# Performance work log

Measured on AMD Instinct MI355X. Metric: run time of the kernel, lower is better.

The kernel has to match this reference:

```python
import jax, jax.numpy as jnp
import numpy as np

B, S, H, C = 256, 256, 768, 150  # batch, seq_len, hidden_size, total class prototypes


def setup_inputs() -> dict:
    key = jax.random.key(0)
    k1, k2, k3 = jax.random.split(key, 3)
    last_hidden_state = jax.random.normal(k1, (B, S, H), dtype=jnp.float32)
    attention_mask = jnp.ones((B, S), dtype=jnp.int32)
    means = jax.random.normal(k2, (C, H), dtype=jnp.float32)
    A = jax.random.normal(k3, (H, H), dtype=jnp.float32) / np.sqrt(H)
    # symmetric PSD-ish inverse-covariance, like pinv of a covariance (hermitian)
    cov_inv = A @ A.T + jnp.eye(H, dtype=jnp.float32)
    return {"last_hidden_state": last_hidden_state, "attention_mask": attention_mask,
            "means": means, "cov_inv": cov_inv}


def reference(last_hidden_state, attention_mask, means, cov_inv):
    # mean pooling over valid tokens: [B, S, H] -> [B, H]
    m = attention_mask[..., None].astype(last_hidden_state.dtype)
    prelogits = (last_hidden_state * m).sum(axis=1) / jnp.clip(m.sum(axis=1), 1e-9, None)
    # mahalanobis score per class, vectorized over all C prototypes:
    xS = prelogits @ cov_inv                      # [B, H]
    t_x = jnp.sum(xS * prelogits, axis=-1)        # [B]
    mS = means @ cov_inv                          # [C, H]
    t_m = jnp.sum(mS * means, axis=-1)            # [C]
    scores = t_x[:, None] - 2.0 * (xS @ means.T) + t_m[None, :]  # [B, C]
    scores_over_tasks = scores.T                  # [C, B], matches torch.stack/cat layout
    indices = jnp.argmin(scores_over_tasks, axis=0)  # [B]
    return indices, scores_over_tasks
```

## Files before the change

### kernel.cpp

```cpp
#include <hip/hip_runtime.h>
#include <hip/hip_bf16.h>

#define B 256
#define S 256
#define H 768
#define C 150
#define H4 192


__global__ __launch_bounds__(768) void kPool(const float* __restrict__ lhs,
                                             const int* __restrict__ mask,
                                             float* __restrict__ prelogits) {
    const int b = blockIdx.x;
    const int t = threadIdx.x;
    const int q = t / H4, c4 = t - q * H4;
    __shared__ float msk[S];
    __shared__ float4 qbuf[3][H4];
    __shared__ float cntsh;

    if (t < S) msk[t] = (float)mask[b * S + t];
    __syncthreads();

    if (t >= 704) {
        const int idx = t - 704;
        float v = msk[idx] + msk[idx + 64] + msk[idx + 128] + msk[idx + 192];
#pragma unroll
        for (int off = 32; off > 0; off >>= 1) v += __shfl_down(v, off, 64);
        if (idx == 0) cntsh = v;
    }

    const float4* src = (const float4*)lhs + (size_t)(b * S + q * 64) * H4 + c4;
    const float* mrow = msk + q * 64;
    float4 acc = make_float4(0.f, 0.f, 0.f, 0.f);
#pragma unroll 8
    for (int s = 0; s < 64; ++s) {
        const float m = mrow[s];
        const float4 v = src[(size_t)s * H4];
        acc.x += v.x * m; acc.y += v.y * m; acc.z += v.z * m; acc.w += v.w * m;
    }
    if (q > 0) qbuf[q - 1][c4] = acc;
    __syncthreads();
    if (q == 0) {
        const float4 a1 = qbuf[0][c4], a2 = qbuf[1][c4], a3 = qbuf[2][c4];
        const float inv = 1.0f / fmaxf(cntsh, 1e-9f);
        float4 r;
        r.x = (acc.x + a1.x + a2.x + a3.x) * inv;
        r.y = (acc.y + a1.y + a2.y + a3.y) * inv;
        r.z = (acc.z + a1.z + a2.z + a3.z) * inv;
        r.w = (acc.w + a1.w + a2.w + a3.w) * inv;
        ((float4*)prelogits)[(size_t)b * H4 + c4] = r;
    }
}

__global__ __launch_bounds__(192) void kC(const float* __restrict__ prelogits,
                                          const float* __restrict__ cov,
                                          const float* __restrict__ means,
                                          float* __restrict__ dp,
                                          float* __restrict__ tx_part,
                                          float* __restrict__ tm_part) {
    const int t = threadIdx.x;
    const int kg = t / 24, c4 = t % 24;
    __shared__ float xsl[8 * H];
    __shared__ float4 red2[8][24];
    __shared__ float4 xsf[8][24];
    __shared__ float sred[8][3];

    if (blockIdx.x < 256) {
        const int rt = blockIdx.x >> 3, cs = blockIdx.x & 7;
        const int r0 = rt * 8, cb = cs * 24;

#pragma unroll
        for (int r = 0; r < 8; ++r)
            ((float4*)xsl)[r * H4 + t] = ((const float4*)prelogits)[(size_t)(r0 + r) * H4 + t];
        __syncthreads();

        float4 acc[8];
#pragma unroll
        for (int r = 0; r < 8; ++r) acc[r] = make_float4(0.f, 0.f, 0.f, 0.f);
        const float4* cov4 = (const float4*)cov + cb + c4;
#pragma unroll 4
        for (int kk = 0; kk < 96; ++kk) {
            const int k = kg * 96 + kk;
            const float4 cv = cov4[(size_t)k * H4];
#pragma unroll
            for (int r = 0; r < 8; ++r) {
                const float xv = xsl[r * H + k];
                acc[r].x += xv * cv.x; acc[r].y += xv * cv.y;
                acc[r].z += xv * cv.z; acc[r].w += xv * cv.w;
            }
        }

        float pdr[8];
#pragma unroll
        for (int r = 0; r < 8; ++r) pdr[r] = 0.f;
        for (int r = 0; r < 8; ++r) {
            red2[kg][c4] = acc[r];
            __syncthreads();
            if (kg == 0) {
                float4 s = red2[0][c4];
#pragma unroll
                for (int g = 1; g < 8; ++g) {
                    const float4 q = red2[g][c4];
                    s.x += q.x; s.y += q.y; s.z += q.z; s.w += q.w;
                }
                xsf[r][c4] = s;
                const float4 xv = ((float4*)xsl)[r * H4 + cb + c4];
                pdr[r] = s.x * xv.x + s.y * xv.y + s.z * xv.z + s.w * xv.w;
            }
            __syncthreads();
        }

        if (t < 64) {
#pragma unroll
            for (int r = 0; r < 8; ++r) {
                float v = (t < 24) ? pdr[r] : 0.f;
#pragma unroll
                for (int off = 16; off > 0; off >>= 1) v += __shfl_down(v, off, 32);
                if (t == 0) tx_part[cs * 256 + r0 + r] = v;
            }
        }

        if (t < C) {
            const float4* mu4 = (const float4*)means + (size_t)t * H4 + cb;
            float a8[8];
#pragma unroll
            for (int r = 0; r < 8; ++r) a8[r] = 0.f;
#pragma unroll 4
            for (int j = 0; j < 24; ++j) {
                const float4 mv = mu4[j];
#pragma unroll
                for (int r = 0; r < 8; ++r) {
                    const float4 x = xsf[r][j];
                    a8[r] += mv.x * x.x + mv.y * x.y + mv.z * x.z + mv.w * x.w;
                }
            }
#pragma unroll
            for (int r = 0; r < 8; ++r)
                dp[((size_t)(cs * 256) + (r0 + r)) * 150 + t] = a8[r];
        }
    } else {
        const int idx = blockIdx.x - 256;
        const int rt = idx >> 3, cs = idx & 7;
        const int r0 = rt * 8, cb = cs * 24;

        for (int r = 0; r < 8; ++r) {
            const int row = r0 + r;
            float4 v = make_float4(0.f, 0.f, 0.f, 0.f);
            if (row < C) v = ((const float4*)means)[(size_t)row * H4 + t];
            ((float4*)xsl)[r * H4 + t] = v;
        }
        __syncthreads();

        float4 acc[8];
#pragma unroll
        for (int r = 0; r < 8; ++r) acc[r] = make_float4(0.f, 0.f, 0.f, 0.f);
        const float4* cov4 = (const float4*)cov + cb + c4;
#pragma unroll 4
        for (int kk = 0; kk < 96; ++kk) {
            const int k = kg * 96 + kk;
            const float4 cv = cov4[(size_t)k * H4];
#pragma unroll
            for (int r = 0; r < 8; ++r) {
                const float xv = xsl[r * H + k];
                acc[r].x += xv * cv.x; acc[r].y += xv * cv.y;
                acc[r].z += xv * cv.z; acc[r].w += xv * cv.w;
            }
        }
        const int w = t >> 6;
#pragma unroll
        for (int r = 0; r < 8; ++r) {
            const float4 mu = ((float4*)xsl)[r * H4 + cb + c4];
            float pd = acc[r].x * mu.x + acc[r].y * mu.y + acc[r].z * mu.z + acc[r].w * mu.w;
#pragma unroll
            for (int off = 32; off > 0; off >>= 1) pd += __shfl_down(pd, off, 64);
            if ((t & 63) == 0) sred[r][w] = pd;
        }
        __syncthreads();
        if (t < 8) {
            const int row = r0 + t;
            if (row < C)
                tm_part[cs * 152 + row] = sred[t][0] + sred[t][1] + sred[t][2];
        }
    }
}

__global__ __launch_bounds__(192) void kD(const float* __restrict__ dp,
                                          const float* __restrict__ tx_part,
                                          const float* __restrict__ tm_part,
                                          float* __restrict__ out) {
    const int b = blockIdx.x, t = threadIdx.x;
    __shared__ float sv[192];
    __shared__ int si[192];

    float sc = INFINITY;
    if (t < C) {
        float d = 0.f;
#pragma unroll
        for (int j = 0; j < 8; ++j) d += dp[((size_t)(j * 256) + b) * 150 + t];
        float tx = 0.f;
#pragma unroll
        for (int j = 0; j < 8; ++j) tx += tx_part[j * 256 + b];
        float tm = 0.f;
#pragma unroll
        for (int j = 0; j < 8; ++j) tm += tm_part[j * 152 + t];
        sc = tx - 2.0f * d + tm;
        out[B + (size_t)t * B + b] = sc;
    }
    sv[t] = sc;
    si[t] = (t < C) ? t : 0x7fffffff;
    __syncthreads();
#pragma unroll
    for (int off = 96; off >= 3; off >>= 1) {
        if (t < off) {
            const float ov = sv[t + off];
            const int oi = si[t + off];
            if (ov < sv[t] || (ov == sv[t] && oi < si[t])) { sv[t] = ov; si[t] = oi; }
        }
        __syncthreads();
    }
    if (t == 0) {
        float bv = sv[0];
        int bi = si[0];
#pragma unroll
        for (int j = 1; j < 3; ++j)
            if (sv[j] < bv || (sv[j] == bv && si[j] < bi)) { bv = sv[j]; bi = si[j]; }
        out[b] = (float)bi;
    }
}

extern "C" void kernel_launch(void* const* d_in, const int* in_sizes, int n_in,
                              void* d_out, int out_size, void* d_ws, size_t ws_size,
                              hipStream_t stream) {
    const float* lhs   = (const float*)d_in[0];
    const int*   mask  = (const int*)d_in[1];
    const float* means = (const float*)d_in[2];
    const float* cov   = (const float*)d_in[3];
    float* out = (float*)d_out;
    char* ws = (char*)d_ws;

    float* prelogits = (float*)(ws + 0);
    float* dp        = (float*)(ws + 786432);
    float* tx_part   = (float*)(ws + 2015232);
    float* tm_part   = (float*)(ws + 2023424);

    kPool<<<dim3(B), 768, 0, stream>>>(lhs, mask, prelogits);
    kC<<<dim3(256 + 152), 192, 0, stream>>>(prelogits, cov, means, dp, tx_part, tm_part);
    kD<<<dim3(256), 192, 0, stream>>>(dp, tx_part, tm_part, out);
}
```

Baseline: 56.61 us.

## Fuse pool, projection and argmin into one cooperative kernel with grid syncs

Merges the three kernels into a single cooperative launch of 256 blocks of 768 threads, separated by grid-wide syncs. This removes two kernel launch boundaries. The covariance projection now splits the K dimension across 32 thread groups instead of 8, which lengthens the shared-memory reduction. The t_m work runs on the first 152 blocks after their x-side work, so it is serialized rather than spread over extra blocks. Grid sync overhead and the heavier per-block phase may offset the launch savings.

```diff
diff --git a/kernel.cpp b/kernel.cpp
--- a/kernel.cpp
+++ b/kernel.cpp
@@ -1,5 +1,8 @@
 #include <hip/hip_runtime.h>
 #include <hip/hip_bf16.h>
+#include <hip/hip_cooperative_groups.h>
+
+namespace cg = cooperative_groups;
 
 #define B 256
 #define S 256
@@ -8,70 +11,73 @@
 #define H4 192
 
 
-__global__ __launch_bounds__(768) void kPool(const float* __restrict__ lhs,
+__global__ __launch_bounds__(768) void kMega(const float* __restrict__ lhs,
                                              const int* __restrict__ mask,
-                                             float* __restrict__ prelogits) {
-    const int b = blockIdx.x;
+                                             const float* __restrict__ means,
+                                             const float* __restrict__ cov,
+                                             float* __restrict__ prelogits,
+                                             float* __restrict__ dp,
+                                             float* __restrict__ tx_part,
+                                             float* __restrict__ tm_part,
+                                             float* __restrict__ out) {
+    cg::grid_group grid = cg::this_grid();
+    const int bid = blockIdx.x;
     const int t = threadIdx.x;
-    const int q = t / H4, c4 = t - q * H4;
+
     __shared__ float msk[S];
     __shared__ float4 qbuf[3][H4];
     __shared__ float cntsh;
-
-    if (t < S) msk[t] = (float)mask[b * S + t];
-    __syncthreads();
-
-    if (t >= 704) {
-        const int idx = t - 704;
-        float v = msk[idx] + msk[idx + 64] + msk[idx + 128] + msk[idx + 192];
-#pragma unroll
-        for (int off = 32; off > 0; off >>= 1) v += __shfl_down(v, off, 64);
-        if (idx == 0) cntsh = v;
-    }
-
-    const float4* src = (const float4*)lhs + (size_t)(b * S + q * 64) * H4 + c4;
-    const float* mrow = msk + q * 64;
-    float4 acc = make_float4(0.f, 0.f, 0.f, 0.f);
+    __shared__ float xsl[8 * H];
+    __shared__ float4 red2[32][24];
+    __shared__ float4 xsf[8][24];
+    __shared__ float sred[8][12];
+    __shared__ float sv[192];
+    __shared__ int si[192];
+
+    {
+        const int b = bid;
+        const int q = t / H4, c4 = t - q * H4;
+        if (t < S) msk[t] = (float)mask[b * S + t];
+        __syncthreads();
+        if (t >= 704) {
+            const int idx = t - 704;
+            float v = msk[idx] + msk[idx + 64] + msk[idx + 128] + msk[idx + 192];
+#pragma unroll
+            for (int off = 32; off > 0; off >>= 1) v += __shfl_down(v, off, 64);
+            if (idx == 0) cntsh = v;
+        }
+        const float4* src = (const float4*)lhs + (size_t)(b * S + q * 64) * H4 + c4;
+        const float* mrow = msk + q * 64;
+        float4 acc = make_float4(0.f, 0.f, 0.f, 0.f);
 #pragma unroll 8
-    for (int s = 0; s < 64; ++s) {
-        const float m = mrow[s];
-        const float4 v = src[(size_t)s * H4];
-        acc.x += v.x * m; acc.y += v.y * m; acc.z += v.z * m; acc.w += v.w * m;
-    }
-    if (q > 0) qbuf[q - 1][c4] = acc;
-    __syncthreads();
-    if (q == 0) {
-        const float4 a1 = qbuf[0][c4], a2 = qbuf[1][c4], a3 = qbuf[2][c4];
-        const float inv = 1.0f / fmaxf(cntsh, 1e-9f);
-        float4 r;
-        r.x = (acc.x + a1.x + a2.x + a3.x) * inv;
-        r.y = (acc.y + a1.y + a2.y + a3.y) * inv;
-        r.z = (acc.z + a1.z + a2.z + a3.z) * inv;
-        r.w = (acc.w + a1.w + a2.w + a3.w) * inv;
-        ((float4*)prelogits)[(size_t)b * H4 + c4] = r;
-    }
-}
-
-__global__ __launch_bounds__(192) void kC(const float* __restrict__ prelogits,
-                                          const float* __restrict__ cov,
-                                          const float* __restrict__ means,
-                                          float* __restrict__ dp,
-                                          float* __restrict__ tx_part,
-                                          float* __restrict__ tm_part) {
-    const int t = threadIdx.x;
-    const int kg = t / 24, c4 = t % 24;
-    __shared__ float xsl[8 * H];
-    __shared__ float4 red2[8][24];
-    __shared__ float4 xsf[8][24];
-    __shared__ float sred[8][3];
-
-    if (blockIdx.x < 256) {
-        const int rt = blockIdx.x >> 3, cs = blockIdx.x & 7;
+        for (int s = 0; s < 64; ++s) {
+            const float m = mrow[s];
+            const float4 v = src[(size_t)s * H4];
+            acc.x += v.x * m; acc.y += v.y * m; acc.z += v.z * m; acc.w += v.w * m;
+        }
+        if (q > 0) qbuf[q - 1][c4] = acc;
+        __syncthreads();
+        if (q == 0) {
+            const float4 a1 = qbuf[0][c4], a2 = qbuf[1][c4], a3 = qbuf[2][c4];
+            const float inv = 1.0f / fmaxf(cntsh, 1e-9f);
+            float4 r;
+            r.x = (acc.x + a1.x + a2.x + a3.x) * inv;
+            r.y = (acc.y + a1.y + a2.y + a3.y) * inv;
+            r.z = (acc.z + a1.z + a2.z + a3.z) * inv;
+            r.w = (acc.w + a1.w + a2.w + a3.w) * inv;
+            ((float4*)prelogits)[(size_t)b * H4 + c4] = r;
+        }
+    }
+    __threadfence();
+    grid.sync();
+
+    {
+        const int rt = bid >> 3, cs = bid & 7;
         const int r0 = rt * 8, cb = cs * 24;
-
-#pragma unroll
-        for (int r = 0; r < 8; ++r)
-            ((float4*)xsl)[r * H4 + t] = ((const float4*)prelogits)[(size_t)(r0 + r) * H4 + t];
+        const int kg = t / 24, c4 = t % 24;
+
+        for (int i = t; i < 8 * H4; i += 768)
+            ((float4*)xsl)[i] = ((const float4*)prelogits)[(size_t)(r0 + i / H4) * H4 + (i % H4)];
         __syncthreads();
 
         float4 acc[8];
@@ -79,8 +85,8 @@
         for (int r = 0; r < 8; ++r) acc[r] = make_float4(0.f, 0.f, 0.f, 0.f);
         const float4* cov4 = (const float4*)cov + cb + c4;
 #pragma unroll 4
-        for (int kk = 0; kk < 96; ++kk) {
-            const int k = kg * 96 + kk;
+        for (int kk = 0; kk < 24; ++kk) {
+            const int k = kg * 24 + kk;
             const float4 cv = cov4[(size_t)k * H4];
 #pragma unroll
             for (int r = 0; r < 8; ++r) {
@@ -99,9 +105,9 @@
             if (kg == 0) {
                 float4 s = red2[0][c4];
 #pragma unroll
-                for (int g = 1; g < 8; ++g) {
-                    const float4 q = red2[g][c4];
-                    s.x += q.x; s.y += q.y; s.z += q.z; s.w += q.w;
+                for (int g = 1; g < 32; ++g) {
+                    const float4 q2 = red2[g][c4];
+                    s.x += q2.x; s.y += q2.y; s.z += q2.z; s.w += q2.w;
                 }
                 xsf[r][c4] = s;
                 const float4 xv = ((float4*)xsl)[r * H4 + cb + c4];
@@ -138,16 +144,19 @@
             for (int r = 0; r < 8; ++r)
                 dp[((size_t)(cs * 256) + (r0 + r)) * 150 + t] = a8[r];
         }
-    } else {
-        const int idx = blockIdx.x - 256;
-        const int rt = idx >> 3, cs = idx & 7;
+    }
+
+    if (bid < 152) {
+        __syncthreads();
+        const int rt = bid >> 3, cs = bid & 7;
         const int r0 = rt * 8, cb = cs * 24;
-
-        for (int r = 0; r < 8; ++r) {
-            const int row = r0 + r;
+        const int kg = t / 24, c4 = t % 24;
+
+        for (int i = t; i < 8 * H4; i += 768) {
+            const int row = r0 + i / H4;
             float4 v = make_float4(0.f, 0.f, 0.f, 0.f);
-            if (row < C) v = ((const float4*)means)[(size_t)row * H4 + t];
-            ((float4*)xsl)[r * H4 + t] = v;
+            if (row < C) v = ((const float4*)means)[(size_t)row * H4 + (i % H4)];
+            ((float4*)xsl)[i] = v;
         }
         __syncthreads();
 
@@ -156,8 +165,8 @@
         for (int r = 0; r < 8; ++r) acc[r] = make_float4(0.f, 0.f, 0.f, 0.f);
         const float4* cov4 = (const float4*)cov + cb + c4;
 #pragma unroll 4
-        for (int kk = 0; kk < 96; ++kk) {
-            const int k = kg * 96 + kk;
+        for (int kk = 0; kk < 24; ++kk) {
+            const int k = kg * 24 + kk;
             const float4 cv = cov4[(size_t)k * H4];
 #pragma unroll
             for (int r = 0; r < 8; ++r) {
@@ -178,53 +187,55 @@
         __syncthreads();
         if (t < 8) {
             const int row = r0 + t;
-            if (row < C)
-                tm_part[cs * 152 + row] = sred[t][0] + sred[t][1] + sred[t][2];
-        }
-    }
-}
-
-__global__ __launch_bounds__(192) void kD(const float* __restrict__ dp,
-                                          const float* __restrict__ tx_part,
-                                          const float* __restrict__ tm_part,
-                                          float* __restrict__ out) {
-    const int b = blockIdx.x, t = threadIdx.x;
-    __shared__ float sv[192];
-    __shared__ int si[192];
-
-    float sc = INFINITY;
-    if (t < C) {
-        float d = 0.f;
-#pragma unroll
-        for (int j = 0; j < 8; ++j) d += dp[((size_t)(j * 256) + b) * 150 + t];
-        float tx = 0.f;
-#pragma unroll
-        for (int j = 0; j < 8; ++j) tx += tx_part[j * 256 + b];
-        float tm = 0.f;
-#pragma unroll
-        for (int j = 0; j < 8; ++j) tm += tm_part[j * 152 + t];
-        sc = tx - 2.0f * d + tm;
-        out[B + (size_t)t * B + b] = sc;
-    }
-    sv[t] = sc;
-    si[t] = (t < C) ? t : 0x7fffffff;
-    __syncthreads();
-#pragma unroll
-    for (int off = 96; off >= 3; off >>= 1) {
-        if (t < off) {
-            const float ov = sv[t + off];
-            const int oi = si[t + off];
-            if (ov < sv[t] || (ov == sv[t] && oi < si[t])) { sv[t] = ov; si[t] = oi; }
-        }
-        __syncthreads();
-    }
-    if (t == 0) {
-        float bv = sv[0];
-        int bi = si[0];
-#pragma unroll
-        for (int j = 1; j < 3; ++j)
-            if (sv[j] < bv || (sv[j] == bv && si[j] < bi)) { bv = sv[j]; bi = si[j]; }
-        out[b] = (float)bi;
+            if (row < C) {
+                float s = 0.f;
+#pragma unroll
+                for (int j = 0; j < 12; ++j) s += sred[t][j];
+                tm_part[cs * 152 + row] = s;
+            }
+        }
+    }
+    __threadfence();
+    grid.sync();
+
+    {
+        const int b = bid;
+        if (t < 192) {
+            float sc = INFINITY;
+            if (t < C) {
+                float d = 0.f;
+#pragma unroll
+                for (int j = 0; j < 8; ++j) d += dp[((size_t)(j * 256) + b) * 150 + t];
+                float tx = 0.f;
+#pragma unroll
+                for (int j = 0; j < 8; ++j) tx += tx_part[j * 256 + b];
+                float tm = 0.f;
+#pragma unroll
+                for (int j = 0; j < 8; ++j) tm += tm_part[j * 152 + t];
+                sc = tx - 2.0f * d + tm;
+                out[B + (size_t)t * B + b] = sc;
+            }
+            sv[t] = sc;
+            si[t] = (t < C) ? t : 0x7fffffff;
+        }
+        __syncthreads();
+#pragma unroll
+        for (int off = 96; off >= 3; off >>= 1) {
+            if (t < off) {
+                const float ov = sv[t + off];
+                const int oi = si[t + off];
+                if (ov < sv[t] || (ov == sv[t] && oi < si[t])) { sv[t] = ov; si[t] = oi; }
+            }
+            __syncthreads();
+        }
+        if (t == 0) {
+            float bv = sv[0];
+            int bi = si[0];
+#pragma unroll
+            for (int j = 1; j < 3; ++j)
+                if (sv[j] < bv || (sv[j] == bv && si[j] < bi)) { bv = sv[j]; bi = si[j]; }
+            out[b] = (float)bi;
+        }
     }
 }
 
@@ -243,7 +254,8 @@
     float* tx_part   = (float*)(ws + 2015232);
     float* tm_part   = (float*)(ws + 2023424);
 
-    kPool<<<dim3(B), 768, 0, stream>>>(lhs, mask, prelogits);
-    kC<<<dim3(256 + 152), 192, 0, stream>>>(prelogits, cov, means, dp, tx_part, tm_part);
-    kD<<<dim3(256), 192, 0, stream>>>(dp, tx_part, tm_part, out);
+    void* args[] = {(void*)&lhs, (void*)&mask, (void*)&means, (void*)&cov,
+                    (void*)&prelogits, (void*)&dp, (void*)&tx_part,
+                    (void*)&tm_part, (void*)&out};
+    hipLaunchCooperativeKernel((void*)kMega, dim3(B), dim3(768), args, 0, stream);
 }
```

New measurement: 216.2 us. 282% more time.
